# Kernel tuning notes

Hardware: AMD Instinct MI355X
Metric: run time of the kernel (lower is better)

Reference implementation:

```python
import jax, jax.numpy as jnp
import numpy as np

# TensorProductConvLayer (DiffDock-style): gather -> edge-MLP-weighted fully
# connected tensor product (lmax=1 irreps) -> scatter-mean.
# in/out irreps: ns x0e + nv x1o + nv x1e + ns x0o ; sh irreps: 1x0e + 1x1o
NS, NV = 16, 4
N_NODES, N_EDGES = 8000, 160000
EDGE_FEAT = 3 * NS                      # 48
IRREPS_DIM = 2 * NS + 6 * NV            # 56
# per-path weight block sizes (fully-connected 'uvw' paths, mul2 = 1):
# [A:0e*0e->0e, B:1o*1o->0e, A:0e*1o->1o, B:1o*0e->1o, C:1e*1o->1o,
#  B:1o*1o->1e, C:1e*0e->1e, D:0o*1o->1e, C:1e*1o->0o, D:0o*0e->0o]
PATH_SIZES = [NS*NS, NV*NS, NS*NV, NV*NV, NV*NV, NV*NV, NV*NV, NS*NV, NV*NS, NS*NS]
W_NUMEL = sum(PATH_SIZES)               # 832
# component-normalized CG factors: 1x1->0 uses delta/sqrt(3); 1x1->1 uses eps/sqrt(2)
INV_SQRT3 = float(1.0 / np.sqrt(3.0))
INV_SQRT2 = float(1.0 / np.sqrt(2.0))
# element path normalization: 1/sqrt(total fan-in mul per output irrep)
A_SCAL = float(1.0 / np.sqrt(NS + NV))      # 0e / 0o outputs
A_VEC = float(1.0 / np.sqrt(NS + 2 * NV))   # 1o / 1e outputs


def setup_inputs() -> dict:
    key = jax.random.key(0)
    ks = jax.random.split(key, 6)
    node_attr = jax.random.normal(ks[0], (N_NODES, IRREPS_DIM), jnp.float32)
    edge_index = jax.random.randint(ks[1], (2, N_EDGES), 0, N_NODES)
    edge_attr = jax.random.normal(ks[2], (N_EDGES, EDGE_FEAT), jnp.float32)
    edge_sh = jax.random.normal(ks[3], (N_EDGES, 4), jnp.float32)
    s = float(1.0 / np.sqrt(EDGE_FEAT))
    fc_w1 = jax.random.normal(ks[4], (EDGE_FEAT, EDGE_FEAT), jnp.float32) * s
    fc_b1 = jnp.zeros((EDGE_FEAT,), jnp.float32)
    fc_w2 = jax.random.normal(ks[5], (EDGE_FEAT, W_NUMEL), jnp.float32) * s
    fc_b2 = jnp.zeros((W_NUMEL,), jnp.float32)
    return dict(node_attr=node_attr, edge_attr=edge_attr, edge_sh=edge_sh,
                fc_w1=fc_w1, fc_b1=fc_b1, fc_w2=fc_w2, fc_b2=fc_b2,
                edge_index=edge_index)


def _split_weights(w):
    outs, off = [], 0
    for sz in PATH_SIZES:
        outs.append(w[:, off:off + sz])
        off += sz
    return outs


def _tp_conv(node_attr, edge_attr, edge_sh, fc_w1, fc_b1, fc_w2, fc_b2, src, dst):
    # edge MLP -> per-edge tensor-product weights [E, 832]
    h = jax.nn.relu(edge_attr @ fc_w1 + fc_b1)
    w = h @ fc_w2 + fc_b2
    wA0, wB0, wA1, wB1, wC1, wB1e, wC1e, wD1e, wC0o, wD0o = _split_weights(w)

    x = node_attr[dst]                         # gather [E, 56]
    x0e = x[:, :NS]
    x1o = x[:, NS:NS + 3 * NV].reshape(-1, NV, 3)
    x1e = x[:, NS + 3 * NV:NS + 6 * NV].reshape(-1, NV, 3)
    x0o = x[:, NS + 6 * NV:]
    s0 = edge_sh[:, 0]
    s1 = edge_sh[:, 1:4]

    # ---- 0e output [E, ns]
    o0e = jnp.einsum('eu,euv->ev', x0e, wA0.reshape(-1, NS, NS)) * s0[:, None]
    dot_b = jnp.einsum('eui,ei->eu', x1o, s1) * INV_SQRT3   # 1o x 1o -> 0e
    o0e = (o0e + jnp.einsum('eu,euv->ev', dot_b, wB0.reshape(-1, NV, NS))) * A_SCAL

    # ---- 1o output [E, nv, 3]
    o1o = jnp.einsum('eu,euv->ev', x0e, wA1.reshape(-1, NS, NV))[:, :, None] * s1[:, None, :]
    o1o = o1o + jnp.einsum('eui,euv->evi', x1o, wB1.reshape(-1, NV, NV)) * s0[:, None, None]
    cr_e = jnp.cross(x1e, s1[:, None, :]) * INV_SQRT2       # 1e x 1o -> 1o
    o1o = (o1o + jnp.einsum('eui,euv->evi', cr_e, wC1.reshape(-1, NV, NV))) * A_VEC

    # ---- 1e output [E, nv, 3]
    cr_o = jnp.cross(x1o, s1[:, None, :]) * INV_SQRT2       # 1o x 1o -> 1e
    o1e = jnp.einsum('eui,euv->evi', cr_o, wB1e.reshape(-1, NV, NV))
    o1e = o1e + jnp.einsum('eui,euv->evi', x1e, wC1e.reshape(-1, NV, NV)) * s0[:, None, None]
    o1e = (o1e + jnp.einsum('eu,euv->ev', x0o, wD1e.reshape(-1, NS, NV))[:, :, None] * s1[:, None, :]) * A_VEC

    # ---- 0o output [E, ns]
    dot_c = jnp.einsum('eui,ei->eu', x1e, s1) * INV_SQRT3   # 1e x 1o -> 0o
    o0o = jnp.einsum('eu,euv->ev', dot_c, wC0o.reshape(-1, NV, NS))
    o0o = (o0o + jnp.einsum('eu,euv->ev', x0o, wD0o.reshape(-1, NS, NS)) * s0[:, None]) * A_SCAL

    tp = jnp.concatenate([o0e, o1o.reshape(-1, 3 * NV), o1e.reshape(-1, 3 * NV), o0o], axis=-1)

    # scatter-mean over source nodes
    summed = jax.ops.segment_sum(tp, src, num_segments=N_NODES)
    counts = jax.ops.segment_sum(jnp.ones((tp.shape[0],), tp.dtype), src, num_segments=N_NODES)
    return summed / jnp.maximum(counts, 1.0)[:, None]


def reference(node_attr, edge_attr, edge_sh, fc_w1, fc_b1, fc_w2, fc_b2, edge_index):
    src, dst = edge_index[0], edge_index[1]
    return _tp_conv(node_attr, edge_attr, edge_sh, fc_w1, fc_b1, fc_w2, fc_b2, src, dst)
```

## Files before the change

kernel.cpp:

```cpp
#include <hip/hip_runtime.h>
#include <hip/hip_fp16.h>

#define IRR    56
#define EF     48
#define WN     832
#define NEDGE  160000
#define NNODE  8000
#define NT     256
#define EB     64
#define NBLK   (NEDGE / EB)
#define NPASS  4
#define TPP    13
#define SW2_U16 (TPP * 2 * 64 * 8)

#define SG_STRIDE 60
#define SH_STRIDE 72
#define SF_STRIDE 120

#define INV_SQRT3 0.5773502691896258f
#define INV_SQRT2 0.7071067811865476f
#define A_SCAL    0.22360679774997896f
#define A_VEC     0.20412414523193154f

typedef __bf16 bf16x8 __attribute__((ext_vector_type(8)));
typedef float  f32x4  __attribute__((ext_vector_type(4)));
typedef unsigned short u16x8 __attribute__((ext_vector_type(8)));
typedef unsigned short u16x4 __attribute__((ext_vector_type(4)));

__device__ __forceinline__ unsigned short f2bf(float f) {
    unsigned int u = __builtin_bit_cast(unsigned int, f);
    u += 0x7FFFu + ((u >> 16) & 1u);
    return (unsigned short)(u >> 16);
}
__device__ __forceinline__ unsigned short f2h(float f) {
    __half h = __float2half(f);
    return __builtin_bit_cast(unsigned short, h);
}
__device__ __forceinline__ float h2f(unsigned short u) {
    __half h = __builtin_bit_cast(__half, u);
    return __half2float(h);
}

__global__ void k_setup(const float* __restrict__ w1, const float* __restrict__ b1,
                        const float* __restrict__ w2, const float* __restrict__ b2,
                        unsigned short* __restrict__ W1T, unsigned short* __restrict__ W2L,
                        float* __restrict__ accum_counts)
{
    int o = blockIdx.x * 256 + threadIdx.x;
    if (o < NNODE * IRR + NNODE) accum_counts[o] = 0.f;
    if (o < 52 * 2 * 64 * 8) {
        int i = o >> 10;
        int rem = o & 1023;
        int f = rem >> 9;
        int rem2 = rem & 511;
        int l = rem2 >> 3, j = rem2 & 7;
        int mm = l & 15, qq = l >> 4;
        int k = f * 32 + qq * 8 + j;
        int n = i * 16 + mm;
        float v = (k < EF) ? w2[k * WN + n] : ((k == EF) ? b2[n] : 0.f);
        W2L[o] = f2bf(v);
    }
    if (o < EF * EF) { int k = o / EF, n = o - k * EF; W1T[n * 64 + k] = f2bf(w1[o]); }
    if (o < EF * 16) { int n = o >> 4, kk = EF + (o & 15); W1T[n * 64 + kk] = (kk == EF) ? f2bf(b1[n]) : (unsigned short)0; }
}

__global__ __launch_bounds__(NT) void tp_fused(
    const float* __restrict__ node_attr,
    const float* __restrict__ edge_attr,
    const float* __restrict__ edge_sh,
    const int*   __restrict__ edge_index,
    const unsigned short* __restrict__ W1T,
    const unsigned short* __restrict__ W2L,
    float* __restrict__ accum,
    float* __restrict__ counts)
{
    __shared__ __align__(16) unsigned short sW2[SW2_U16];
    __shared__ __align__(16) unsigned short sH[EB * SH_STRIDE];
    __shared__ __align__(16) unsigned short sF[EB * SF_STRIDE];
    __shared__ float sS1[EB][4];
    __shared__ int   sSrc[EB], sDst[EB];

    const int tid  = threadIdx.x;
    const int lane = tid & 63;
    const int wv   = tid >> 6;
    const int m    = lane & 15;
    const int quad = lane >> 4;
    const int e0   = blockIdx.x * EB;
    const int em   = wv * 16 + m;
    const int ew0  = e0 + wv * 16;

    if (tid < EB)            sSrc[tid]       = edge_index[e0 + tid];
    else if (tid < 2 * EB)   sDst[tid - EB]  = edge_index[NEDGE + e0 + tid - EB];
    __syncthreads();

    float* sG = (float*)sW2;
    {
        const float* nrow = node_attr + (size_t)sDst[em] * IRR;
        float* g = sG + em * SG_STRIDE;
        #pragma unroll
        for (int t = 0; t < 3; t++) {
            int c = quad + t * 4;
            *(float4*)(g + c * 4) = *(const float4*)(nrow + c * 4);
        }
        if (quad < 2) { int c = 12 + quad; *(float4*)(g + c * 4) = *(const float4*)(nrow + c * 4); }
    }

    {
        const float* arow = edge_attr + (size_t)(ew0 + m) * EF;
        float av0[8], av1[8];
        {
            float4 p0 = *(const float4*)(arow + quad * 8);
            float4 p1 = *(const float4*)(arow + quad * 8 + 4);
            av0[0]=p0.x; av0[1]=p0.y; av0[2]=p0.z; av0[3]=p0.w;
            av0[4]=p1.x; av0[5]=p1.y; av0[6]=p1.z; av0[7]=p1.w;
        }
        if (quad < 2) {
            float4 p0 = *(const float4*)(arow + 32 + quad * 8);
            float4 p1 = *(const float4*)(arow + 32 + quad * 8 + 4);
            av1[0]=p0.x; av1[1]=p0.y; av1[2]=p0.z; av1[3]=p0.w;
            av1[4]=p1.x; av1[5]=p1.y; av1[6]=p1.z; av1[7]=p1.w;
        } else {
            #pragma unroll
            for (int j = 0; j < 8; j++) av1[j] = 0.f;
            if (quad == 2) av1[0] = 1.f;
        }
        u16x8 ub0, ub1;
        #pragma unroll
        for (int j = 0; j < 8; j++) { ub0[j] = f2bf(av0[j]); ub1[j] = f2bf(av1[j]); }
        bf16x8 hb0 = __builtin_bit_cast(bf16x8, ub0);
        bf16x8 hb1 = __builtin_bit_cast(bf16x8, ub1);

        #pragma unroll
        for (int nth = 0; nth < 3; nth++) {
            bf16x8 a0 = __builtin_bit_cast(bf16x8, *(const u16x8*)&W1T[(nth*16 + m)*64 + quad*8]);
            bf16x8 a1 = __builtin_bit_cast(bf16x8, *(const u16x8*)&W1T[(nth*16 + m)*64 + 32 + quad*8]);
            f32x4 c = {0.f, 0.f, 0.f, 0.f};
            c = __builtin_amdgcn_mfma_f32_16x16x32_bf16(a0, hb0, c, 0, 0, 0);
            c = __builtin_amdgcn_mfma_f32_16x16x32_bf16(a1, hb1, c, 0, 0, 0);
            u16x4 hp;
            #pragma unroll
            for (int r = 0; r < 4; r++) hp[r] = f2bf(fmaxf(c[r], 0.f));
            *(u16x4*)&sH[em * SH_STRIDE + nth*16 + quad*4] = hp;
        }
        if (quad == 3) {
            u16x4 b = {0x3F80, 0, 0, 0}, z = {0, 0, 0, 0};
            *(u16x4*)&sH[em * SH_STRIDE + 48] = b;
            *(u16x4*)&sH[em * SH_STRIDE + 52] = z;
            *(u16x4*)&sH[em * SH_STRIDE + 56] = z;
            *(u16x4*)&sH[em * SH_STRIDE + 60] = z;
        }
    }
    __syncthreads();

    if (quad == 0) {
        const float* x = sG + em * SG_STRIDE;
        float4 sh4 = *(const float4*)&edge_sh[(size_t)(ew0 + m) * 4];
        const float s0 = sh4.x, sx = sh4.y, sy = sh4.z, sz = sh4.w;
        unsigned short* F = sF + em * SF_STRIDE;
        const float c0S = s0 * A_SCAL;
        const float c0V = s0 * A_VEC;
        const float cD3 = INV_SQRT3 * A_SCAL;
        const float cC2 = INV_SQRT2 * A_VEC;
        #pragma unroll
        for (int u = 0; u < 16; u++) {
            float x0e = x[u], x0o = x[40 + u];
            F[u]       = f2h(x0e * c0S);
            F[20 + u]  = f2h(x0e * A_VEC);
            F[84 + u]  = f2h(x0o * A_VEC);
            F[104 + u] = f2h(x0o * c0S);
        }
        #pragma unroll
        for (int u = 0; u < 4; u++) {
            float a0 = x[16 + u*3], a1 = x[16 + u*3 + 1], a2 = x[16 + u*3 + 2];
            float b0 = x[28 + u*3], b1 = x[28 + u*3 + 1], b2 = x[28 + u*3 + 2];
            F[16 + u]  = f2h((a0*sx + a1*sy + a2*sz) * cD3);
            F[100 + u] = f2h((b0*sx + b1*sy + b2*sz) * cD3);
            F[48 + u*3 + 0] = f2h((b1*sz - b2*sy) * cC2);
            F[48 + u*3 + 1] = f2h((b2*sx - b0*sz) * cC2);
            F[48 + u*3 + 2] = f2h((b0*sy - b1*sx) * cC2);
            F[60 + u*3 + 0] = f2h((a1*sz - a2*sy) * cC2);
            F[60 + u*3 + 1] = f2h((a2*sx - a0*sz) * cC2);
            F[60 + u*3 + 2] = f2h((a0*sy - a1*sx) * cC2);
            F[36 + u*3 + 0] = f2h(a0 * c0V);  F[36 + u*3 + 1] = f2h(a1 * c0V);  F[36 + u*3 + 2] = f2h(a2 * c0V);
            F[72 + u*3 + 0] = f2h(b0 * c0V);  F[72 + u*3 + 1] = f2h(b1 * c0V);  F[72 + u*3 + 2] = f2h(b2 * c0V);
        }
        sS1[em][0] = sx; sS1[em][1] = sy; sS1[em][2] = sz;
    }
    __syncthreads();

    bf16x8 HB0 = __builtin_bit_cast(bf16x8, *(const u16x8*)&sH[em * SH_STRIDE + quad*8]);
    bf16x8 HB1 = __builtin_bit_cast(bf16x8, *(const u16x8*)&sH[em * SH_STRIDE + 32 + quad*8]);
    __syncthreads();

    float oe[4]  = {0.f,0.f,0.f,0.f};
    float oo[4]  = {0.f,0.f,0.f,0.f};
    float sA[4]  = {0.f,0.f,0.f,0.f};
    float sD[4]  = {0.f,0.f,0.f,0.f};
    float t1o[12] = {0.f,0.f,0.f,0.f,0.f,0.f,0.f,0.f,0.f,0.f,0.f,0.f};
    float t1e[12] = {0.f,0.f,0.f,0.f,0.f,0.f,0.f,0.f,0.f,0.f,0.f,0.f};

    const unsigned short* Fm = sF + em * SF_STRIDE;

    auto consume = [&](int nt, f32x4 c) {
        if (nt < 20) {
            float f = h2f(Fm[nt]);
            #pragma unroll
            for (int r = 0; r < 4; r++) oe[r] += f * c[r];
        } else if (nt < 24) {
            float f = h2f(Fm[20 + (nt - 20)*4 + quad]);
            #pragma unroll
            for (int r = 0; r < 4; r++) sA[r] += f * c[r];
        } else if (nt < 26) {
            int u = (nt - 24)*4 + quad;
            #pragma unroll
            for (int i = 0; i < 3; i++) {
                float f = h2f(Fm[36 + u*3 + i]);
                #pragma unroll
                for (int r = 0; r < 4; r++) t1o[i*4 + r] += f * c[r];
            }
        } else if (nt < 28) {
            int j = (nt - 26)*4 + quad;
            #pragma unroll
            for (int i = 0; i < 3; i++) {
                float f = h2f(Fm[60 + j*3 + i]);
                #pragma unroll
                for (int r = 0; r < 4; r++) t1e[i*4 + r] += f * c[r];
            }
        } else if (nt < 32) {
            float f = h2f(Fm[84 + (nt - 28)*4 + quad]);
            #pragma unroll
            for (int r = 0; r < 4; r++) sD[r] += f * c[r];
        } else {
            float f = h2f(Fm[68 + nt]);
            #pragma unroll
            for (int r = 0; r < 4; r++) oo[r] += f * c[r];
        }
    };

    const uint4* w2src = (const uint4*)W2L;
    uint4* w2dst = (uint4*)sW2;

    #pragma unroll 1
    for (int p = 0; p < NPASS; p++) {
        __syncthreads();
        {
            const uint4* src = w2src + p * 1664;
            #pragma unroll
            for (int it = 0; it < 7; it++) {
                int idx = it * 256 + tid;
                if (idx < 1664) w2dst[idx] = src[idx];
            }
        }
        __syncthreads();

        #pragma unroll
        for (int i = 0; i < TPP; i++) {
            u16x8 A = *(const u16x8*)&sW2[i * 1024 + lane * 8];
            u16x8 B = *(const u16x8*)&sW2[i * 1024 + 512 + lane * 8];
            f32x4 c = {0.f, 0.f, 0.f, 0.f};
            c = __builtin_amdgcn_mfma_f32_16x16x32_bf16(__builtin_bit_cast(bf16x8, A), HB0, c, 0, 0, 0);
            c = __builtin_amdgcn_mfma_f32_16x16x32_bf16(__builtin_bit_cast(bf16x8, B), HB1, c, 0, 0, 0);
            consume(p * TPP + i, c);
        }
    }

    #pragma unroll
    for (int r = 0; r < 4; r++) {
        sA[r] += __shfl_xor(sA[r], 16, 64);  sA[r] += __shfl_xor(sA[r], 32, 64);
        sD[r] += __shfl_xor(sD[r], 16, 64);  sD[r] += __shfl_xor(sD[r], 32, 64);
    }
    #pragma unroll
    for (int i = 0; i < 12; i++) {
        t1o[i] += __shfl_xor(t1o[i], 16, 64);  t1o[i] += __shfl_xor(t1o[i], 32, 64);
        t1e[i] += __shfl_xor(t1e[i], 16, 64);  t1e[i] += __shfl_xor(t1e[i], 32, 64);
    }

    __syncthreads();

    float* sO = (float*)sF;
    {
        float4 v0; v0.x = oe[0]; v0.y = oe[1]; v0.z = oe[2]; v0.w = oe[3];
        float4 v1; v1.x = oo[0]; v1.y = oo[1]; v1.z = oo[2]; v1.w = oo[3];
        *(float4*)&sO[em * 60 + quad*4]      = v0;
        *(float4*)&sO[em * 60 + 40 + quad*4] = v1;
    }
    if (quad == 0) {
        float s1x = sS1[em][0], s1y = sS1[em][1], s1z = sS1[em][2];
        #pragma unroll
        for (int r = 0; r < 4; r++) {
            sO[em * 60 + 16 + r*3 + 0] = sA[r] * s1x + t1o[0*4 + r];
            sO[em * 60 + 16 + r*3 + 1] = sA[r] * s1y + t1o[1*4 + r];
            sO[em * 60 + 16 + r*3 + 2] = sA[r] * s1z + t1o[2*4 + r];
        }
    } else if (quad == 1) {
        float s1x = sS1[em][0], s1y = sS1[em][1], s1z = sS1[em][2];
        #pragma unroll
        for (int r = 0; r < 4; r++) {
            sO[em * 60 + 28 + r*3 + 0] = sD[r] * s1x + t1e[0*4 + r];
            sO[em * 60 + 28 + r*3 + 1] = sD[r] * s1y + t1e[1*4 + r];
            sO[em * 60 + 28 + r*3 + 2] = sD[r] * s1z + t1e[2*4 + r];
        }
    }
    __syncthreads();

    #pragma unroll
    for (int it = 0; it < 14; it++) {
        int idx = it * NT + tid;
        int e = idx / IRR, ch = idx - e * IRR;
        unsafeAtomicAdd(&accum[(size_t)sSrc[e] * IRR + ch], sO[e * 60 + ch]);
    }
    if (tid < EB) unsafeAtomicAdd(&counts[sSrc[tid]], 1.0f);
}

__global__ void tp_divide(const float* __restrict__ accum,
                          const float* __restrict__ counts,
                          float* __restrict__ out)
{
    int idx = blockIdx.x * blockDim.x + threadIdx.x;
    if (idx < NNODE * IRR) {
        out[idx] = accum[idx] / fmaxf(counts[idx / IRR], 1.0f);
    }
}

extern "C" void kernel_launch(void* const* d_in, const int* in_sizes, int n_in,
                              void* d_out, int out_size, void* d_ws, size_t ws_size,
                              hipStream_t stream) {
    const float* node_attr  = (const float*)d_in[0];
    const float* edge_attr  = (const float*)d_in[1];
    const float* edge_sh    = (const float*)d_in[2];
    const float* fc_w1      = (const float*)d_in[3];
    const float* fc_b1      = (const float*)d_in[4];
    const float* fc_w2      = (const float*)d_in[5];
    const float* fc_b2      = (const float*)d_in[6];
    const int*   edge_index = (const int*)d_in[7];

    float* accum  = (float*)d_ws;
    float* counts = accum + (size_t)NNODE * IRR;
    unsigned short* W1T = (unsigned short*)(counts + NNODE);
    unsigned short* W2L = W1T + EF * 64;

    k_setup<<<(NNODE * IRR + NNODE + 255) / 256, 256, 0, stream>>>(
        fc_w1, fc_b1, fc_w2, fc_b2, W1T, W2L, accum);

    tp_fused<<<NBLK, NT, 0, stream>>>(node_attr, edge_attr, edge_sh, edge_index,
                                      W1T, W2L, accum, counts);

    tp_divide<<<(NNODE * IRR + 255) / 256, 256, 0, stream>>>(accum, counts, (float*)d_out);
}
```

Baseline: 192.4 us.

## Persistent blocks split W2 paths by output half with resident weights and prescaled scatter

Changes tp_fused into a persistent kernel with 512 blocks. Each block belongs to one of two flavors: the flavors cover the 0e/1o outputs or the 1e/0o outputs. A block loads its half of the bf16 W2 tiles (26 tiles) into LDS once and loops over 64-edge tasks, so W2 is no longer reloaded in four passes per block. The in-degree histogram is computed in the setup kernel, and each edge's contribution is scaled by 1/count before the atomic add straight into the output, which removes the separate divide kernel and the count atomics. In exchange, each flavor block repeats the first MLP layer and the node gathers. Splitting the work also duplicates per-edge preprocessing, and the larger LDS footprint may limit occupancy.

New measurement: 176.2 us. 8.5% less time.

```diff
diff --git a/kernel.cpp b/kernel.cpp
--- a/kernel.cpp
+++ b/kernel.cpp
@@ -7,15 +7,9 @@
 #define NEDGE  160000
 #define NNODE  8000
 #define NT     256
-#define EB     64
-#define NBLK   (NEDGE / EB)
-#define NPASS  4
-#define TPP    13
-#define SW2_U16 (TPP * 2 * 64 * 8)
-
-#define SG_STRIDE 60
-#define SH_STRIDE 72
-#define SF_STRIDE 120
+#define TE2    64
+#define NTASK  (NEDGE / TE2)
+#define GRID   512
 
 #define INV_SQRT3 0.5773502691896258f
 #define INV_SQRT2 0.7071067811865476f
@@ -44,10 +38,9 @@
 __global__ void k_setup(const float* __restrict__ w1, const float* __restrict__ b1,
                         const float* __restrict__ w2, const float* __restrict__ b2,
                         unsigned short* __restrict__ W1T, unsigned short* __restrict__ W2L,
-                        float* __restrict__ accum_counts)
+                        const int* __restrict__ edge_index, int* __restrict__ hist)
 {
     int o = blockIdx.x * 256 + threadIdx.x;
-    if (o < NNODE * IRR + NNODE) accum_counts[o] = 0.f;
     if (o < 52 * 2 * 64 * 8) {
         int i = o >> 10;
         int rem = o & 1023;
@@ -62,263 +55,281 @@
     }
     if (o < EF * EF) { int k = o / EF, n = o - k * EF; W1T[n * 64 + k] = f2bf(w1[o]); }
     if (o < EF * 16) { int n = o >> 4, kk = EF + (o & 15); W1T[n * 64 + kk] = (kk == EF) ? f2bf(b1[n]) : (unsigned short)0; }
-}
-
-__global__ __launch_bounds__(NT) void tp_fused(
+    if (o < NEDGE) atomicAdd(&hist[edge_index[o]], 1);
+}
+
+__global__ __launch_bounds__(NT, 2) void tp_fused(
     const float* __restrict__ node_attr,
     const float* __restrict__ edge_attr,
     const float* __restrict__ edge_sh,
     const int*   __restrict__ edge_index,
+    const int*   __restrict__ hist,
     const unsigned short* __restrict__ W1T,
     const unsigned short* __restrict__ W2L,
-    float* __restrict__ accum,
-    float* __restrict__ counts)
+    float* __restrict__ out)
 {
-    __shared__ __align__(16) unsigned short sW2[SW2_U16];
-    __shared__ __align__(16) unsigned short sH[EB * SH_STRIDE];
-    __shared__ __align__(16) unsigned short sF[EB * SF_STRIDE];
-    __shared__ float sS1[EB][4];
-    __shared__ int   sSrc[EB], sDst[EB];
-
-    const int tid  = threadIdx.x;
-    const int lane = tid & 63;
-    const int wv   = tid >> 6;
-    const int m    = lane & 15;
-    const int quad = lane >> 4;
-    const int e0   = blockIdx.x * EB;
-    const int em   = wv * 16 + m;
-    const int ew0  = e0 + wv * 16;
-
-    if (tid < EB)            sSrc[tid]       = edge_index[e0 + tid];
-    else if (tid < 2 * EB)   sDst[tid - EB]  = edge_index[NEDGE + e0 + tid - EB];
-    __syncthreads();
-
-    float* sG = (float*)sW2;
+    __shared__ __align__(16) unsigned short sW2[26 * 1024];
+    __shared__ __align__(16) unsigned char  UGH[TE2 * 56 * 4];
+    __shared__ __align__(16) unsigned char  UFO[TE2 * 60 * 2];
+    __shared__ float sS1[TE2][4];
+    __shared__ int   sSrc[TE2], sDst[TE2];
+    __shared__ float sInv[TE2];
+
+    float*          sG   = (float*)UGH;
+    unsigned short* sH   = (unsigned short*)UGH;
+    unsigned short* sF16 = (unsigned short*)UFO;
+    float*          sO   = (float*)UFO;
+
+    const int tid    = threadIdx.x;
+    const int lane   = tid & 63;
+    const int wv     = tid >> 6;
+    const int m      = lane & 15;
+    const int quad   = lane >> 4;
+    const int em     = wv * 16 + m;
+    const int flavor = blockIdx.x & 1;
+    const int bid2   = blockIdx.x >> 1;
+
     {
-        const float* nrow = node_attr + (size_t)sDst[em] * IRR;
-        float* g = sG + em * SG_STRIDE;
+        const uint4* src = (const uint4*)(W2L + (size_t)flavor * 26 * 1024);
+        uint4* dst = (uint4*)sW2;
         #pragma unroll
-        for (int t = 0; t < 3; t++) {
-            int c = quad + t * 4;
-            *(float4*)(g + c * 4) = *(const float4*)(nrow + c * 4);
-        }
-        if (quad < 2) { int c = 12 + quad; *(float4*)(g + c * 4) = *(const float4*)(nrow + c * 4); }
+        for (int it = 0; it < 13; it++) dst[it * NT + tid] = src[it * NT + tid];
     }
 
-    {
-        const float* arow = edge_attr + (size_t)(ew0 + m) * EF;
-        float av0[8], av1[8];
+    for (int task = bid2; task < NTASK; task += 256) {
+        const int e0 = task * TE2;
+        __syncthreads();
+        if (tid < TE2)            sSrc[tid]       = edge_index[e0 + tid];
+        else if (tid < 2 * TE2)   sDst[tid - TE2] = edge_index[NEDGE + e0 + tid - TE2];
+        __syncthreads();
+
         {
-            float4 p0 = *(const float4*)(arow + quad * 8);
-            float4 p1 = *(const float4*)(arow + quad * 8 + 4);
-            av0[0]=p0.x; av0[1]=p0.y; av0[2]=p0.z; av0[3]=p0.w;
-            av0[4]=p1.x; av0[5]=p1.y; av0[6]=p1.z; av0[7]=p1.w;
-        }
-        if (quad < 2) {
-            float4 p0 = *(const float4*)(arow + 32 + quad * 8);
-            float4 p1 = *(const float4*)(arow + 32 + quad * 8 + 4);
-            av1[0]=p0.x; av1[1]=p0.y; av1[2]=p0.z; av1[3]=p0.w;
-            av1[4]=p1.x; av1[5]=p1.y; av1[6]=p1.z; av1[7]=p1.w;
+            const float* nrow = node_attr + (size_t)sDst[em] * IRR;
+            float* g = sG + em * 56;
+            #pragma unroll
+            for (int t = 0; t < 3; t++) {
+                int c = quad + t * 4;
+                *(float4*)(g + c * 4) = *(const float4*)(nrow + c * 4);
+            }
+            if (quad < 2) { int c = 12 + quad; *(float4*)(g + c * 4) = *(const float4*)(nrow + c * 4); }
+        }
+        if (tid >= 128 && tid < 128 + TE2) {
+            int e = tid - 128;
+            sInv[e] = 1.0f / fmaxf((float)hist[sSrc[e]], 1.0f);
+        }
+        __syncthreads();
+
+        if (quad == 0) {
+            const float* x = sG + em * 56;
+            float4 sh4 = *(const float4*)&edge_sh[(size_t)(e0 + em) * 4];
+            const float s0 = sh4.x, sx = sh4.y, sy = sh4.z, sz = sh4.w;
+            unsigned short* F = sF16 + em * 60;
+            const float c0S = s0 * A_SCAL;
+            const float c0V = s0 * A_VEC;
+            const float cD3 = INV_SQRT3 * A_SCAL;
+            const float cC2 = INV_SQRT2 * A_VEC;
+            if (flavor == 0) {
+                #pragma unroll
+                for (int u = 0; u < 16; u++) {
+                    float x0e = x[u];
+                    F[u]      = f2h(x0e * c0S);
+                    F[20 + u] = f2h(x0e * A_VEC);
+                }
+                #pragma unroll
+                for (int u = 0; u < 4; u++) {
+                    float a0 = x[16 + u*3], a1 = x[16 + u*3 + 1], a2 = x[16 + u*3 + 2];
+                    float b0 = x[28 + u*3], b1 = x[28 + u*3 + 1], b2 = x[28 + u*3 + 2];
+                    F[16 + u] = f2h((a0*sx + a1*sy + a2*sz) * cD3);
+                    F[36 + u*3 + 0] = f2h(a0 * c0V);
+                    F[36 + u*3 + 1] = f2h(a1 * c0V);
+                    F[36 + u*3 + 2] = f2h(a2 * c0V);
+                    F[48 + u*3 + 0] = f2h((b1*sz - b2*sy) * cC2);
+                    F[48 + u*3 + 1] = f2h((b2*sx - b0*sz) * cC2);
+                    F[48 + u*3 + 2] = f2h((b0*sy - b1*sx) * cC2);
+                }
+            } else {
+                #pragma unroll
+                for (int u = 0; u < 4; u++) {
+                    float a0 = x[16 + u*3], a1 = x[16 + u*3 + 1], a2 = x[16 + u*3 + 2];
+                    float b0 = x[28 + u*3], b1 = x[28 + u*3 + 1], b2 = x[28 + u*3 + 2];
+                    F[u*3 + 0]      = f2h((a1*sz - a2*sy) * cC2);
+                    F[u*3 + 1]      = f2h((a2*sx - a0*sz) * cC2);
+                    F[u*3 + 2]      = f2h((a0*sy - a1*sx) * cC2);
+                    F[12 + u*3 + 0] = f2h(b0 * c0V);
+                    F[12 + u*3 + 1] = f2h(b1 * c0V);
+                    F[12 + u*3 + 2] = f2h(b2 * c0V);
+                    F[40 + u]       = f2h((b0*sx + b1*sy + b2*sz) * cD3);
+                }
+                #pragma unroll
+                for (int u = 0; u < 16; u++) {
+                    float x0o = x[40 + u];
+                    F[24 + u] = f2h(x0o * A_VEC);
+                    F[44 + u] = f2h(x0o * c0S);
+                }
+            }
+            sS1[em][0] = sx; sS1[em][1] = sy; sS1[em][2] = sz;
+        }
+        __syncthreads();
+
+        {
+            const float* arow = edge_attr + (size_t)(e0 + em) * EF;
+            float av0[8], av1[8];
+            {
+                float4 p0 = *(const float4*)(arow + quad * 8);
+                float4 p1 = *(const float4*)(arow + quad * 8 + 4);
+                av0[0]=p0.x; av0[1]=p0.y; av0[2]=p0.z; av0[3]=p0.w;
+                av0[4]=p1.x; av0[5]=p1.y; av0[6]=p1.z; av0[7]=p1.w;
+            }
+            if (quad < 2) {
+                float4 p0 = *(const float4*)(arow + 32 + quad * 8);
+                float4 p1 = *(const float4*)(arow + 32 + quad * 8 + 4);
+                av1[0]=p0.x; av1[1]=p0.y; av1[2]=p0.z; av1[3]=p0.w;
+                av1[4]=p1.x; av1[5]=p1.y; av1[6]=p1.z; av1[7]=p1.w;
+            } else {
+                #pragma unroll
+                for (int j = 0; j < 8; j++) av1[j] = 0.f;
+                if (quad == 2) av1[0] = 1.f;
+            }
+            u16x8 ub0, ub1;
+            #pragma unroll
+            for (int j = 0; j < 8; j++) { ub0[j] = f2bf(av0[j]); ub1[j] = f2bf(av1[j]); }
+            bf16x8 hb0 = __builtin_bit_cast(bf16x8, ub0);
+            bf16x8 hb1 = __builtin_bit_cast(bf16x8, ub1);
+
+            #pragma unroll
+            for (int nth = 0; nth < 3; nth++) {
+                bf16x8 a0 = __builtin_bit_cast(bf16x8, *(const u16x8*)&W1T[(nth*16 + m)*64 + quad*8]);
+                bf16x8 a1 = __builtin_bit_cast(bf16x8, *(const u16x8*)&W1T[(nth*16 + m)*64 + 32 + quad*8]);
+                f32x4 c = {0.f, 0.f, 0.f, 0.f};
+                c = __builtin_amdgcn_mfma_f32_16x16x32_bf16(a0, hb0, c, 0, 0, 0);
+                c = __builtin_amdgcn_mfma_f32_16x16x32_bf16(a1, hb1, c, 0, 0, 0);
+                u16x4 hp;
+                #pragma unroll
+                for (int r = 0; r < 4; r++) hp[r] = f2bf(fmaxf(c[r], 0.f));
+                *(u16x4*)&sH[em * 72 + nth*16 + quad*4] = hp;
+            }
+            if (quad == 3) {
+                u16x4 b = {0x3F80, 0, 0, 0}, z = {0, 0, 0, 0};
+                *(u16x4*)&sH[em * 72 + 48] = b;
+                *(u16x4*)&sH[em * 72 + 52] = z;
+                *(u16x4*)&sH[em * 72 + 56] = z;
+                *(u16x4*)&sH[em * 72 + 60] = z;
+            }
+        }
+        __syncthreads();
+
+        bf16x8 HB0 = __builtin_bit_cast(bf16x8, *(const u16x8*)&sH[em * 72 + quad*8]);
+        bf16x8 HB1 = __builtin_bit_cast(bf16x8, *(const u16x8*)&sH[em * 72 + 32 + quad*8]);
+
+        const unsigned short* Fp = sF16 + em * 60;
+        const float s1x = sS1[em][0], s1y = sS1[em][1], s1z = sS1[em][2];
+
+        if (flavor == 0) {
+            float oe[4] = {0.f,0.f,0.f,0.f};
+            float sA[4] = {0.f,0.f,0.f,0.f};
+            float t1[12] = {0.f,0.f,0.f,0.f,0.f,0.f,0.f,0.f,0.f,0.f,0.f,0.f};
+            #pragma unroll
+            for (int i = 0; i < 26; i++) {
+                u16x8 Af = *(const u16x8*)&sW2[i * 1024 + lane * 8];
+                u16x8 Bf = *(const u16x8*)&sW2[i * 1024 + 512 + lane * 8];
+                f32x4 c = {0.f,0.f,0.f,0.f};
+                c = __builtin_amdgcn_mfma_f32_16x16x32_bf16(__builtin_bit_cast(bf16x8, Af), HB0, c, 0, 0, 0);
+                c = __builtin_amdgcn_mfma_f32_16x16x32_bf16(__builtin_bit_cast(bf16x8, Bf), HB1, c, 0, 0, 0);
+                if (i < 20) {
+                    float f = h2f(Fp[i]);
+                    #pragma unroll
+                    for (int r = 0; r < 4; r++) oe[r] += f * c[r];
+                } else if (i < 24) {
+                    float f = h2f(Fp[20 + (i - 20)*4 + quad]);
+                    #pragma unroll
+                    for (int r = 0; r < 4; r++) sA[r] += f * c[r];
+                } else {
+                    int u = (i - 24)*4 + quad;
+                    #pragma unroll
+                    for (int i3 = 0; i3 < 3; i3++) {
+                        float f = h2f(Fp[36 + u*3 + i3]);
+                        #pragma unroll
+                        for (int r = 0; r < 4; r++) t1[i3*4 + r] += f * c[r];
+                    }
+                }
+            }
+            #pragma unroll
+            for (int r = 0; r < 4; r++) {
+                sA[r] += __shfl_xor(sA[r], 16, 64);  sA[r] += __shfl_xor(sA[r], 32, 64);
+            }
+            #pragma unroll
+            for (int i = 0; i < 12; i++) {
+                t1[i] += __shfl_xor(t1[i], 16, 64);  t1[i] += __shfl_xor(t1[i], 32, 64);
+            }
+            __syncthreads();
+            float4 v0; v0.x = oe[0]; v0.y = oe[1]; v0.z = oe[2]; v0.w = oe[3];
+            *(float4*)&sO[em * 28 + quad*4] = v0;
+            if (quad == 0) {
+                #pragma unroll
+                for (int r = 0; r < 4; r++) {
+                    sO[em * 28 + 16 + r*3 + 0] = sA[r] * s1x + t1[0*4 + r];
+                    sO[em * 28 + 16 + r*3 + 1] = sA[r] * s1y + t1[1*4 + r];
+                    sO[em * 28 + 16 + r*3 + 2] = sA[r] * s1z + t1[2*4 + r];
+                }
+            }
         } else {
-            #pragma unroll
-            for (int j = 0; j < 8; j++) av1[j] = 0.f;
-            if (quad == 2) av1[0] = 1.f;
-        }
-        u16x8 ub0, ub1;
+            float sD[4] = {0.f,0.f,0.f,0.f};
+            float t1[12] = {0.f,0.f,0.f,0.f,0.f,0.f,0.f,0.f,0.f,0.f,0.f,0.f};
+            float oo[4] = {0.f,0.f,0.f,0.f};
+            #pragma unroll
+            for (int i = 0; i < 26; i++) {
+                u16x8 Af = *(const u16x8*)&sW2[i * 1024 + lane * 8];
+                u16x8 Bf = *(const u16x8*)&sW2[i * 1024 + 512 + lane * 8];
+                f32x4 c = {0.f,0.f,0.f,0.f};
+                c = __builtin_amdgcn_mfma_f32_16x16x32_bf16(__builtin_bit_cast(bf16x8, Af), HB0, c, 0, 0, 0);
+                c = __builtin_amdgcn_mfma_f32_16x16x32_bf16(__builtin_bit_cast(bf16x8, Bf), HB1, c, 0, 0, 0);
+                if (i < 2) {
+                    int j = i*4 + quad;
+                    #pragma unroll
+                    for (int i3 = 0; i3 < 3; i3++) {
+                        float f = h2f(Fp[j*3 + i3]);
+                        #pragma unroll
+                        for (int r = 0; r < 4; r++) t1[i3*4 + r] += f * c[r];
+                    }
+                } else if (i < 6) {
+                    float f = h2f(Fp[24 + (i - 2)*4 + quad]);
+                    #pragma unroll
+                    for (int r = 0; r < 4; r++) sD[r] += f * c[r];
+                } else {
+                    float f = h2f(Fp[40 + (i - 6)]);
+                    #pragma unroll
+                    for (int r = 0; r < 4; r++) oo[r] += f * c[r];
+                }
+            }
+            #pragma unroll
+            for (int r = 0; r < 4; r++) {
+                sD[r] += __shfl_xor(sD[r], 16, 64);  sD[r] += __shfl_xor(sD[r], 32, 64);
+            }
+            #pragma unroll
+            for (int i = 0; i < 12; i++) {
+                t1[i] += __shfl_xor(t1[i], 16, 64);  t1[i] += __shfl_xor(t1[i], 32, 64);
+            }
+            __syncthreads();
+            float4 v1; v1.x = oo[0]; v1.y = oo[1]; v1.z = oo[2]; v1.w = oo[3];
+            *(float4*)&sO[em * 28 + 12 + quad*4] = v1;
+            if (quad == 0) {
+                #pragma unroll
+                for (int r = 0; r < 4; r++) {
+                    sO[em * 28 + r*3 + 0] = sD[r] * s1x + t1[0*4 + r];
+                    sO[em * 28 + r*3 + 1] = sD[r] * s1y + t1[1*4 + r];
+                    sO[em * 28 + r*3 + 2] = sD[r] * s1z + t1[2*4 + r];
+                }
+            }
+        }
+        __syncthreads();
+
         #pragma unroll
-        for (int j = 0; j < 8; j++) { ub0[j] = f2bf(av0[j]); ub1[j] = f2bf(av1[j]); }
-        bf16x8 hb0 = __builtin_bit_cast(bf16x8, ub0);
-        bf16x8 hb1 = __builtin_bit_cast(bf16x8, ub1);
-
-        #pragma unroll
-        for (int nth = 0; nth < 3; nth++) {
-            bf16x8 a0 = __builtin_bit_cast(bf16x8, *(const u16x8*)&W1T[(nth*16 + m)*64 + quad*8]);
-            bf16x8 a1 = __builtin_bit_cast(bf16x8, *(const u16x8*)&W1T[(nth*16 + m)*64 + 32 + quad*8]);
-            f32x4 c = {0.f, 0.f, 0.f, 0.f};
-            c = __builtin_amdgcn_mfma_f32_16x16x32_bf16(a0, hb0, c, 0, 0, 0);
-            c = __builtin_amdgcn_mfma_f32_16x16x32_bf16(a1, hb1, c, 0, 0, 0);
-            u16x4 hp;
-            #pragma unroll
-            for (int r = 0; r < 4; r++) hp[r] = f2bf(fmaxf(c[r], 0.f));
-            *(u16x4*)&sH[em * SH_STRIDE + nth*16 + quad*4] = hp;
-        }
-        if (quad == 3) {
-            u16x4 b = {0x3F80, 0, 0, 0}, z = {0, 0, 0, 0};
-            *(u16x4*)&sH[em * SH_STRIDE + 48] = b;
-            *(u16x4*)&sH[em * SH_STRIDE + 52] = z;
-            *(u16x4*)&sH[em * SH_STRIDE + 56] = z;
-            *(u16x4*)&sH[em * SH_STRIDE + 60] = z;
-        }
-    }
-    __syncthreads();
-
-    if (quad == 0) {
-        const float* x = sG + em * SG_STRIDE;
-        float4 sh4 = *(const float4*)&edge_sh[(size_t)(ew0 + m) * 4];
-        const float s0 = sh4.x, sx = sh4.y, sy = sh4.z, sz = sh4.w;
-        unsigned short* F = sF + em * SF_STRIDE;
-        const float c0S = s0 * A_SCAL;
-        const float c0V = s0 * A_VEC;
-        const float cD3 = INV_SQRT3 * A_SCAL;
-        const float cC2 = INV_SQRT2 * A_VEC;
-        #pragma unroll
-        for (int u = 0; u < 16; u++) {
-            float x0e = x[u], x0o = x[40 + u];
-            F[u]       = f2h(x0e * c0S);
-            F[20 + u]  = f2h(x0e * A_VEC);
-            F[84 + u]  = f2h(x0o * A_VEC);
-            F[104 + u] = f2h(x0o * c0S);
-        }
-        #pragma unroll
-        for (int u = 0; u < 4; u++) {
-            float a0 = x[16 + u*3], a1 = x[16 + u*3 + 1], a2 = x[16 + u*3 + 2];
-            float b0 = x[28 + u*3], b1 = x[28 + u*3 + 1], b2 = x[28 + u*3 + 2];
-            F[16 + u]  = f2h((a0*sx + a1*sy + a2*sz) * cD3);
-            F[100 + u] = f2h((b0*sx + b1*sy + b2*sz) * cD3);
-            F[48 + u*3 + 0] = f2h((b1*sz - b2*sy) * cC2);
-            F[48 + u*3 + 1] = f2h((b2*sx - b0*sz) * cC2);
-            F[48 + u*3 + 2] = f2h((b0*sy - b1*sx) * cC2);
-            F[60 + u*3 + 0] = f2h((a1*sz - a2*sy) * cC2);
-            F[60 + u*3 + 1] = f2h((a2*sx - a0*sz) * cC2);
-            F[60 + u*3 + 2] = f2h((a0*sy - a1*sx) * cC2);
-            F[36 + u*3 + 0] = f2h(a0 * c0V);  F[36 + u*3 + 1] = f2h(a1 * c0V);  F[36 + u*3 + 2] = f2h(a2 * c0V);
-            F[72 + u*3 + 0] = f2h(b0 * c0V);  F[72 + u*3 + 1] = f2h(b1 * c0V);  F[72 + u*3 + 2] = f2h(b2 * c0V);
-        }
-        sS1[em][0] = sx; sS1[em][1] = sy; sS1[em][2] = sz;
-    }
-    __syncthreads();
-
-    bf16x8 HB0 = __builtin_bit_cast(bf16x8, *(const u16x8*)&sH[em * SH_STRIDE + quad*8]);
-    bf16x8 HB1 = __builtin_bit_cast(bf16x8, *(const u16x8*)&sH[em * SH_STRIDE + 32 + quad*8]);
-    __syncthreads();
-
-    float oe[4]  = {0.f,0.f,0.f,0.f};
-    float oo[4]  = {0.f,0.f,0.f,0.f};
-    float sA[4]  = {0.f,0.f,0.f,0.f};
-    float sD[4]  = {0.f,0.f,0.f,0.f};
-    float t1o[12] = {0.f,0.f,0.f,0.f,0.f,0.f,0.f,0.f,0.f,0.f,0.f,0.f};
-    float t1e[12] = {0.f,0.f,0.f,0.f,0.f,0.f,0.f,0.f,0.f,0.f,0.f,0.f};
-
-    const unsigned short* Fm = sF + em * SF_STRIDE;
-
-    auto consume = [&](int nt, f32x4 c) {
-        if (nt < 20) {
-            float f = h2f(Fm[nt]);
-            #pragma unroll
-            for (int r = 0; r < 4; r++) oe[r] += f * c[r];
-        } else if (nt < 24) {
-            float f = h2f(Fm[20 + (nt - 20)*4 + quad]);
-            #pragma unroll
-            for (int r = 0; r < 4; r++) sA[r] += f * c[r];
-        } else if (nt < 26) {
-            int u = (nt - 24)*4 + quad;
-            #pragma unroll
-            for (int i = 0; i < 3; i++) {
-                float f = h2f(Fm[36 + u*3 + i]);
-                #pragma unroll
-                for (int r = 0; r < 4; r++) t1o[i*4 + r] += f * c[r];
-            }
-        } else if (nt < 28) {
-            int j = (nt - 26)*4 + quad;
-            #pragma unroll
-            for (int i = 0; i < 3; i++) {
-                float f = h2f(Fm[60 + j*3 + i]);
-                #pragma unroll
-                for (int r = 0; r < 4; r++) t1e[i*4 + r] += f * c[r];
-            }
-        } else if (nt < 32) {
-            float f = h2f(Fm[84 + (nt - 28)*4 + quad]);
-            #pragma unroll
-            for (int r = 0; r < 4; r++) sD[r] += f * c[r];
-        } else {
-            float f = h2f(Fm[68 + nt]);
-            #pragma unroll
-            for (int r = 0; r < 4; r++) oo[r] += f * c[r];
-        }
-    };
-
-    const uint4* w2src = (const uint4*)W2L;
-    uint4* w2dst = (uint4*)sW2;
-
-    #pragma unroll 1
-    for (int p = 0; p < NPASS; p++) {
-        __syncthreads();
-        {
-            const uint4* src = w2src + p * 1664;
-            #pragma unroll
-            for (int it = 0; it < 7; it++) {
-                int idx = it * 256 + tid;
-                if (idx < 1664) w2dst[idx] = src[idx];
-            }
-        }
-        __syncthreads();
-
-        #pragma unroll
-        for (int i = 0; i < TPP; i++) {
-            u16x8 A = *(const u16x8*)&sW2[i * 1024 + lane * 8];
-            u16x8 B = *(const u16x8*)&sW2[i * 1024 + 512 + lane * 8];
-            f32x4 c = {0.f, 0.f, 0.f, 0.f};
-            c = __builtin_amdgcn_mfma_f32_16x16x32_bf16(__builtin_bit_cast(bf16x8, A), HB0, c, 0, 0, 0);
-            c = __builtin_amdgcn_mfma_f32_16x16x32_bf16(__builtin_bit_cast(bf16x8, B), HB1, c, 0, 0, 0);
-            consume(p * TPP + i, c);
-        }
-    }
-
-    #pragma unroll
-    for (int r = 0; r < 4; r++) {
-        sA[r] += __shfl_xor(sA[r], 16, 64);  sA[r] += __shfl_xor(sA[r], 32, 64);
-        sD[r] += __shfl_xor(sD[r], 16, 64);  sD[r] += __shfl_xor(sD[r], 32, 64);
-    }
-    #pragma unroll
-    for (int i = 0; i < 12; i++) {
-        t1o[i] += __shfl_xor(t1o[i], 16, 64);  t1o[i] += __shfl_xor(t1o[i], 32, 64);
-        t1e[i] += __shfl_xor(t1e[i], 16, 64);  t1e[i] += __shfl_xor(t1e[i], 32, 64);
-    }
-
-    __syncthreads();
-
-    float* sO = (float*)sF;
-    {
-        float4 v0; v0.x = oe[0]; v0.y = oe[1]; v0.z = oe[2]; v0.w = oe[3];
-        float4 v1; v1.x = oo[0]; v1.y = oo[1]; v1.z = oo[2]; v1.w = oo[3];
-        *(float4*)&sO[em * 60 + quad*4]      = v0;
-        *(float4*)&sO[em * 60 + 40 + quad*4] = v1;
-    }
-    if (quad == 0) {
-        float s1x = sS1[em][0], s1y = sS1[em][1], s1z = sS1[em][2];
-        #pragma unroll
-        for (int r = 0; r < 4; r++) {
-            sO[em * 60 + 16 + r*3 + 0] = sA[r] * s1x + t1o[0*4 + r];
-            sO[em * 60 + 16 + r*3 + 1] = sA[r] * s1y + t1o[1*4 + r];
-            sO[em * 60 + 16 + r*3 + 2] = sA[r] * s1z + t1o[2*4 + r];
-        }
-    } else if (quad == 1) {
-        float s1x = sS1[em][0], s1y = sS1[em][1], s1z = sS1[em][2];
-        #pragma unroll
-        for (int r = 0; r < 4; r++) {
-            sO[em * 60 + 28 + r*3 + 0] = sD[r] * s1x + t1e[0*4 + r];
-            sO[em * 60 + 28 + r*3 + 1] = sD[r] * s1y + t1e[1*4 + r];
-            sO[em * 60 + 28 + r*3 + 2] = sD[r] * s1z + t1e[2*4 + r];
-        }
-    }
-    __syncthreads();
-
-    #pragma unroll
-    for (int it = 0; it < 14; it++) {
-        int idx = it * NT + tid;
-        int e = idx / IRR, ch = idx - e * IRR;
-        unsafeAtomicAdd(&accum[(size_t)sSrc[e] * IRR + ch], sO[e * 60 + ch]);
-    }
-    if (tid < EB) unsafeAtomicAdd(&counts[sSrc[tid]], 1.0f);
-}
-
-__global__ void tp_divide(const float* __restrict__ accum,
-                          const float* __restrict__ counts,
-                          float* __restrict__ out)
-{
-    int idx = blockIdx.x * blockDim.x + threadIdx.x;
-    if (idx < NNODE * IRR) {
-        out[idx] = accum[idx] / fmaxf(counts[idx / IRR], 1.0f);
+        for (int it = 0; it < 7; it++) {
+            int idx = it * NT + tid;
+            int e = idx / 28, ch = idx - e * 28;
+            unsafeAtomicAdd(&out[(size_t)sSrc[e] * IRR + flavor * 28 + ch],
+                            sO[e * 28 + ch] * sInv[e]);
+        }
     }
 }
 
@@ -334,16 +345,16 @@
     const float* fc_b2      = (const float*)d_in[6];
     const int*   edge_index = (const int*)d_in[7];
 
-    float* accum  = (float*)d_ws;
-    float* counts = accum + (size_t)NNODE * IRR;
-    unsigned short* W1T = (unsigned short*)(counts + NNODE);
+    int* hist = (int*)d_ws;
+    unsigned short* W1T = (unsigned short*)(hist + NNODE);
     unsigned short* W2L = W1T + EF * 64;
 
-    k_setup<<<(NNODE * IRR + NNODE + 255) / 256, 256, 0, stream>>>(
-        fc_w1, fc_b1, fc_w2, fc_b2, W1T, W2L, accum);
-
-    tp_fused<<<NBLK, NT, 0, stream>>>(node_attr, edge_attr, edge_sh, edge_index,
-                                      W1T, W2L, accum, counts);
-
-    tp_divide<<<(NNODE * IRR + 255) / 256, 256, 0, stream>>>(accum, counts, (float*)d_out);
-}
+    hipMemsetAsync(hist, 0, NNODE * sizeof(int), stream);
+    hipMemsetAsync(d_out, 0, (size_t)out_size * sizeof(float), stream);
+
+    k_setup<<<(NEDGE + 255) / 256, 256, 0, stream>>>(
+        fc_w1, fc_b1, fc_w2, fc_b2, W1T, W2L, edge_index, hist);
+
+    tp_fused<<<GRID, NT, 0, stream>>>(node_attr, edge_attr, edge_sh, edge_index,
+                                      hist, W1T, W2L, (float*)d_out);
+}
```
